# Kernel optimization log

Hardware: AMD Instinct MI355X
Metric: run time of the kernel (lower is better)

## Reference

```python
import jax, jax.numpy as jnp
import numpy as np

EPS = 1e-3
FORGET_BIAS = 1.0


def layer_norm_groups(hmat, n_groups, num_units, gamma, beta):
    # hmat: [B, n_groups*num_units]; normalize each group of num_units independently
    B = hmat.shape[0]
    hr = hmat.reshape(B, n_groups, num_units)
    mean = hr.mean(axis=2, keepdims=True)
    var = ((hr - mean) ** 2).mean(axis=2, keepdims=True)
    hr = (hr - mean) * jax.lax.rsqrt(var + EPS)
    return gamma * hr.reshape(B, n_groups * num_units) + beta


def setup_inputs() -> dict:
    key = jax.random.key(0)
    ks = jax.random.split(key, 5)
    B, I, H = 8192, 1024, 1024
    return {
        "x": jax.random.normal(ks[0], (B, I), jnp.float32),
        "c": jax.random.normal(ks[1], (B, H), jnp.float32),
        "h": jax.random.normal(ks[2], (B, H), jnp.float32),
        "W_xh": jax.random.normal(ks[3], (I, 4 * H), jnp.float32) / np.sqrt(I),
        "W_hh": jax.random.normal(ks[4], (H, 4 * H), jnp.float32) / np.sqrt(H),
        "bias": jnp.zeros((4 * H,), jnp.float32),
        "ln_gamma": jnp.ones((4 * H,), jnp.float32),
        "ln_beta": jnp.zeros((4 * H,), jnp.float32),
        "ln_c_gamma": jnp.ones((H,), jnp.float32),
        "ln_c_beta": jnp.zeros((H,), jnp.float32),
    }


def reference(x, c, h, W_xh, W_hh, bias, ln_gamma, ln_beta, ln_c_gamma, ln_c_beta):
    H = c.shape[1]
    # fused gate matmul: cat([x,h]) @ cat([W_xh,W_hh]) == x@W_xh + h@W_hh
    concat = x @ W_xh + h @ W_hh + bias  # [B, 4H]
    concat = layer_norm_groups(concat, 4, H, ln_gamma, ln_beta)
    i, j, f, o = jnp.split(concat, 4, axis=1)
    new_c = c * jax.nn.sigmoid(f + FORGET_BIAS) + jax.nn.sigmoid(i) * jnp.tanh(j)
    c_ln = layer_norm_groups(new_c, 1, H, ln_c_gamma, ln_c_beta)
    new_h = jnp.tanh(c_ln) * jax.nn.sigmoid(o)
    return new_h, new_c
```

## Files before the change

### kernel.cpp

```cpp
#include <hip/hip_runtime.h>
#include <stdint.h>

#define Mdim 8192
#define Ndim 4096
#define Kdim 2048
#define Hdim 1024

typedef __attribute__((ext_vector_type(8))) short bf16x8;
typedef __attribute__((ext_vector_type(4))) float f32x4;

__device__ __forceinline__ unsigned short f2bf(float f) {
  union { float f; unsigned u; } v; v.f = f;
  unsigned u = v.u + 0x7fffu + ((v.u >> 16) & 1u);
  return (unsigned short)(u >> 16);
}
__device__ __forceinline__ float bf2f(unsigned short s) {
  union { unsigned u; float f; } v; v.u = ((unsigned)s) << 16;
  return v.f;
}
__device__ __forceinline__ float sigmoidf_(float x) { return 1.f / (1.f + __expf(-x)); }
__device__ __forceinline__ float tanhf_(float x) { return 1.f - 2.f / (1.f + __expf(2.f * x)); }

__global__ void conv_a_kernel(const float* __restrict__ x, const float* __restrict__ h,
                              unsigned short* __restrict__ A) {
  int idx = blockIdx.x * 256 + threadIdx.x;
  int m = idx >> 8;
  int k = (idx & 255) * 8;
  const float* src = (k < Hdim) ? (x + (size_t)m * Hdim + k)
                                : (h + (size_t)m * Hdim + (k - Hdim));
  float4 a = ((const float4*)src)[0];
  float4 b = ((const float4*)src)[1];
  union { unsigned short s[8]; int4 v; } o;
  o.s[0] = f2bf(a.x); o.s[1] = f2bf(a.y); o.s[2] = f2bf(a.z); o.s[3] = f2bf(a.w);
  o.s[4] = f2bf(b.x); o.s[5] = f2bf(b.y); o.s[6] = f2bf(b.z); o.s[7] = f2bf(b.w);
  *(int4*)(A + (size_t)idx * 8) = o.v;
}

__global__ void conv_w_kernel(const float* __restrict__ Wxh, const float* __restrict__ Whh,
                              unsigned short* __restrict__ Wt) {
  __shared__ float tile[32][33];
  int k0 = blockIdx.x * 32;
  int n0 = blockIdx.y * 32;
  int tx = threadIdx.x & 31, ty = threadIdx.x >> 5;
#pragma unroll
  for (int i = 0; i < 32; i += 8) {
    int k = k0 + ty + i;
    float v = (k < Hdim) ? Wxh[(size_t)k * Ndim + n0 + tx]
                         : Whh[(size_t)(k - Hdim) * Ndim + n0 + tx];
    tile[ty + i][tx] = v;
  }
  __syncthreads();
#pragma unroll
  for (int i = 0; i < 32; i += 8) {
    int n = n0 + ty + i;
    Wt[(size_t)n * Kdim + k0 + tx] = f2bf(tile[tx][ty + i]);
  }
}

#define BM 128
#define BN 128
#define BK 32
#define NT (Kdim / BK)

__global__ __launch_bounds__(256, 3)
void gemm_kernel(const unsigned short* __restrict__ A, const unsigned short* __restrict__ Bt,
                 unsigned short* __restrict__ C) {
  __shared__ unsigned short lds[2][2][BM * BK];
  int tid = threadIdx.x;
  int bid = blockIdx.x;
  int id = (bid & 7) * 256 + (bid >> 3);
  int mT = id >> 5, nT = id & 31;
  size_t m0 = (size_t)mT * BM, n0 = (size_t)nT * BN;
  int lane = tid & 63, w = tid >> 6;
  int wm = w >> 1, wn = w & 1;
  int q = lane >> 4, r = lane & 15;

  const unsigned short* gA = A + m0 * Kdim;
  const unsigned short* gB = Bt + n0 * Kdim;

  auto stage = [&](int buf, int kt) {
    int k0 = kt * BK;
#pragma unroll
    for (int it = 0; it < 2; ++it) {
      int c = it * 256 + tid;
      int row = c >> 2, slot = c & 3;
      int k8 = slot ^ (row & 3);
      __builtin_amdgcn_global_load_lds(
          (const __attribute__((address_space(1))) void*)(gA + (size_t)row * Kdim + k0 + k8 * 8),
          (__attribute__((address_space(3))) void*)(&lds[buf][0][c * 8]), 16, 0, 0);
      __builtin_amdgcn_global_load_lds(
          (const __attribute__((address_space(1))) void*)(gB + (size_t)row * Kdim + k0 + k8 * 8),
          (__attribute__((address_space(3))) void*)(&lds[buf][1][c * 8]), 16, 0, 0);
    }
  };

  f32x4 acc[4][4] = {};

  stage(0, 0);
  __syncthreads();
  for (int kt = 0; kt < NT; ++kt) {
    int cur = kt & 1;
    if (kt + 1 < NT) stage(cur ^ 1, kt + 1);
    const unsigned short* lA = lds[cur][0];
    const unsigned short* lB = lds[cur][1];
    bf16x8 av[4], bv[4];
    int sl = q ^ (r & 3);
#pragma unroll
    for (int mi = 0; mi < 4; ++mi)
      av[mi] = *(const bf16x8*)(lA + (wm * 64 + mi * 16 + r) * BK + sl * 8);
#pragma unroll
    for (int ni = 0; ni < 4; ++ni)
      bv[ni] = *(const bf16x8*)(lB + (wn * 64 + ni * 16 + r) * BK + sl * 8);
#pragma unroll
    for (int mi = 0; mi < 4; ++mi)
#pragma unroll
      for (int ni = 0; ni < 4; ++ni)
        acc[mi][ni] = __builtin_amdgcn_mfma_f32_16x16x32_bf16(av[mi], bv[ni], acc[mi][ni], 0, 0, 0);
    __syncthreads();
  }

#pragma unroll
  for (int mi = 0; mi < 4; ++mi) {
#pragma unroll
    for (int ni = 0; ni < 4; ++ni) {
      size_t row = m0 + wm * 64 + mi * 16 + q * 4;
      size_t col = n0 + wn * 64 + ni * 16 + r;
#pragma unroll
      for (int j = 0; j < 4; ++j)
        C[(row + j) * Ndim + col] = f2bf(acc[mi][ni][j]);
    }
  }
}

__global__ __launch_bounds__(256)
void tail_kernel(const unsigned short* __restrict__ Cc, const float* __restrict__ cin,
                 const float* __restrict__ bias, const float* __restrict__ gamma,
                 const float* __restrict__ beta, const float* __restrict__ cg,
                 const float* __restrict__ cb, float* __restrict__ out) {
  int lane = threadIdx.x & 63;
  int wid = threadIdx.x >> 6;
  int row = blockIdx.x * 4 + wid;
  const int base = lane * 16;

  const float4* cp = (const float4*)(cin + (size_t)row * Hdim + base);
  float4 c0 = cp[0], c1 = cp[1], c2 = cp[2], c3 = cp[3];
  float cv[16] = {c0.x, c0.y, c0.z, c0.w, c1.x, c1.y, c1.z, c1.w,
                  c2.x, c2.y, c2.z, c2.w, c3.x, c3.y, c3.z, c3.w};

  float accv[16];
  float ov[16];

#pragma unroll
  for (int g = 0; g < 4; ++g) {
    const int4* pp = (const int4*)(Cc + (size_t)row * Ndim + g * Hdim + base);
    int4 u0 = pp[0], u1 = pp[1];
    float vals[16];
    {
      int uu[8] = {u0.x, u0.y, u0.z, u0.w, u1.x, u1.y, u1.z, u1.w};
#pragma unroll
      for (int i = 0; i < 8; ++i) {
        vals[2 * i]     = bf2f((unsigned short)(uu[i] & 0xffff));
        vals[2 * i + 1] = bf2f((unsigned short)(((unsigned)uu[i]) >> 16));
      }
    }
    const float* bp = bias + g * Hdim + base;
#pragma unroll
    for (int t = 0; t < 16; ++t) vals[t] += bp[t];
    float s = 0.f, ss = 0.f;
#pragma unroll
    for (int t = 0; t < 16; ++t) { s += vals[t]; ss += vals[t] * vals[t]; }
#pragma unroll
    for (int off = 32; off; off >>= 1) { s += __shfl_xor(s, off); ss += __shfl_xor(ss, off); }
    float mean = s * (1.f / 1024.f);
    float rstd = rsqrtf(ss * (1.f / 1024.f) - mean * mean + 1e-3f);
    const float* gp = gamma + g * Hdim + base;
    const float* bb = beta + g * Hdim + base;
    if (g == 0) {
#pragma unroll
      for (int t = 0; t < 16; ++t)
        accv[t] = sigmoidf_((vals[t] - mean) * rstd * gp[t] + bb[t]);
    } else if (g == 1) {
#pragma unroll
      for (int t = 0; t < 16; ++t)
        accv[t] *= tanhf_((vals[t] - mean) * rstd * gp[t] + bb[t]);
    } else if (g == 2) {
#pragma unroll
      for (int t = 0; t < 16; ++t)
        accv[t] = cv[t] * sigmoidf_((vals[t] - mean) * rstd * gp[t] + bb[t] + 1.f) + accv[t];
    } else {
#pragma unroll
      for (int t = 0; t < 16; ++t)
        ov[t] = sigmoidf_((vals[t] - mean) * rstd * gp[t] + bb[t]);
    }
  }

  float s = 0.f, ss = 0.f;
#pragma unroll
  for (int t = 0; t < 16; ++t) { s += accv[t]; ss += accv[t] * accv[t]; }
#pragma unroll
  for (int off = 32; off; off >>= 1) { s += __shfl_xor(s, off); ss += __shfl_xor(ss, off); }
  float mean = s * (1.f / 1024.f);
  float rstd = rsqrtf(ss * (1.f / 1024.f) - mean * mean + 1e-3f);

  const float* cgp = cg + base;
  const float* cbp = cb + base;
  float hv[16];
#pragma unroll
  for (int t = 0; t < 16; ++t) {
    float cl = (accv[t] - mean) * rstd * cgp[t] + cbp[t];
    hv[t] = tanhf_(cl) * ov[t];
  }

  float4* oh = (float4*)(out + (size_t)row * Hdim + base);
  float4* oc = (float4*)(out + (size_t)Mdim * Hdim + (size_t)row * Hdim + base);
#pragma unroll
  for (int v = 0; v < 4; ++v) {
    oh[v] = make_float4(hv[4 * v], hv[4 * v + 1], hv[4 * v + 2], hv[4 * v + 3]);
    oc[v] = make_float4(accv[4 * v], accv[4 * v + 1], accv[4 * v + 2], accv[4 * v + 3]);
  }
}

extern "C" void kernel_launch(void* const* d_in, const int* in_sizes, int n_in,
                              void* d_out, int out_size, void* d_ws, size_t ws_size,
                              hipStream_t stream) {
  const float* x    = (const float*)d_in[0];
  const float* c    = (const float*)d_in[1];
  const float* h    = (const float*)d_in[2];
  const float* Wxh  = (const float*)d_in[3];
  const float* Whh  = (const float*)d_in[4];
  const float* bias = (const float*)d_in[5];
  const float* lng  = (const float*)d_in[6];
  const float* lnb  = (const float*)d_in[7];
  const float* cg   = (const float*)d_in[8];
  const float* cb   = (const float*)d_in[9];
  float* out = (float*)d_out;

  unsigned short* Abf = (unsigned short*)d_ws;
  unsigned short* Wt  = Abf + (size_t)Mdim * Kdim;
  unsigned short* Cc  = Wt  + (size_t)Ndim * Kdim;

  conv_a_kernel<<<8192, 256, 0, stream>>>(x, h, Abf);
  conv_w_kernel<<<dim3(Kdim / 32, Ndim / 32), 256, 0, stream>>>(Wxh, Whh, Wt);
  gemm_kernel<<<(Mdim / BM) * (Ndim / BN), 256, 0, stream>>>(Abf, Wt, Cc);
  tail_kernel<<<Mdim / 4, 256, 0, stream>>>(Cc, c, bias, lng, lnb, cg, cb, out);
}
```

Measured before the change: 256.7 us.

## Enlarge GEMM tile to 256x256x64 with 8 waves and interleaved load/MFMA pipeline

Grows the GEMM block tile from 128x128x32 to 256x256x64 and runs it with 512 threads (8 waves). Global-to-LDS staging is split into four quarter regions and interleaved with four MFMA quads per k-step, using barriers, explicit vmcnt waits and s_setprio. The goal is more data reuse per LDS byte and better overlap of memory traffic with matrix math. In exchange it uses more LDS and registers per block and a more fragile hand-written barrier schedule.

```diff
diff --git a/kernel.cpp b/kernel.cpp
--- a/kernel.cpp
+++ b/kernel.cpp
@@ -57,74 +57,148 @@
   }
 }
 
-#define BM 128
-#define BN 128
-#define BK 32
+#define BM 256
+#define BN 256
+#define BK 64
 #define NT (Kdim / BK)
 
-__global__ __launch_bounds__(256, 3)
+__global__ __launch_bounds__(512, 2)
 void gemm_kernel(const unsigned short* __restrict__ A, const unsigned short* __restrict__ Bt,
                  unsigned short* __restrict__ C) {
   __shared__ unsigned short lds[2][2][BM * BK];
-  int tid = threadIdx.x;
+  const int tid = threadIdx.x;
   int bid = blockIdx.x;
-  int id = (bid & 7) * 256 + (bid >> 3);
-  int mT = id >> 5, nT = id & 31;
+  int id = (bid & 7) * 64 + (bid >> 3);
+  int mT = id >> 4, nT = id & 15;
   size_t m0 = (size_t)mT * BM, n0 = (size_t)nT * BN;
-  int lane = tid & 63, w = tid >> 6;
-  int wm = w >> 1, wn = w & 1;
-  int q = lane >> 4, r = lane & 15;
+  const int lane = tid & 63, w = tid >> 6;
+  const int wm = w >> 2, wn = w & 3;
+  const int r16 = lane & 15, q = lane >> 4;
 
   const unsigned short* gA = A + m0 * Kdim;
   const unsigned short* gB = Bt + n0 * Kdim;
 
-  auto stage = [&](int buf, int kt) {
-    int k0 = kt * BK;
+  auto stage = [&](int b, int kt, int region) {
+    const int mat = region >> 1, half = region & 1;
+    const unsigned short* g = mat ? gB : gA;
 #pragma unroll
     for (int it = 0; it < 2; ++it) {
-      int c = it * 256 + tid;
-      int row = c >> 2, slot = c & 3;
-      int k8 = slot ^ (row & 3);
+      int c = it * 512 + tid;
+      int rr = c >> 3, ss = c & 7;
       __builtin_amdgcn_global_load_lds(
-          (const __attribute__((address_space(1))) void*)(gA + (size_t)row * Kdim + k0 + k8 * 8),
-          (__attribute__((address_space(3))) void*)(&lds[buf][0][c * 8]), 16, 0, 0);
-      __builtin_amdgcn_global_load_lds(
-          (const __attribute__((address_space(1))) void*)(gB + (size_t)row * Kdim + k0 + k8 * 8),
-          (__attribute__((address_space(3))) void*)(&lds[buf][1][c * 8]), 16, 0, 0);
+          (const __attribute__((address_space(1))) void*)(
+              g + (size_t)(half * 128 + rr) * Kdim + kt * BK + ((ss ^ (rr & 7)) << 3)),
+          (__attribute__((address_space(3))) void*)(&lds[b][mat][half * (128 * BK) + c * 8]),
+          16, 0, 0);
     }
   };
 
-  f32x4 acc[4][4] = {};
-
-  stage(0, 0);
-  __syncthreads();
-  for (int kt = 0; kt < NT; ++kt) {
-    int cur = kt & 1;
-    if (kt + 1 < NT) stage(cur ^ 1, kt + 1);
-    const unsigned short* lA = lds[cur][0];
-    const unsigned short* lB = lds[cur][1];
-    bf16x8 av[4], bv[4];
-    int sl = q ^ (r & 3);
-#pragma unroll
-    for (int mi = 0; mi < 4; ++mi)
-      av[mi] = *(const bf16x8*)(lA + (wm * 64 + mi * 16 + r) * BK + sl * 8);
-#pragma unroll
-    for (int ni = 0; ni < 4; ++ni)
-      bv[ni] = *(const bf16x8*)(lB + (wn * 64 + ni * 16 + r) * BK + sl * 8);
-#pragma unroll
-    for (int mi = 0; mi < 4; ++mi)
-#pragma unroll
-      for (int ni = 0; ni < 4; ++ni)
-        acc[mi][ni] = __builtin_amdgcn_mfma_f32_16x16x32_bf16(av[mi], bv[ni], acc[mi][ni], 0, 0, 0);
-    __syncthreads();
-  }
-
-#pragma unroll
-  for (int mi = 0; mi < 4; ++mi) {
+  f32x4 acc[8][4] = {};
+  bf16x8 av0[4][2], av1[4][2], bv0[2][2], bv1[2][2];
+
+  auto readA = [&](int cur, int mh, bf16x8 (&av)[4][2]) {
+#pragma unroll
+    for (int mi = 0; mi < 4; ++mi) {
+      int lr = wm * 128 + mh * 64 + mi * 16 + r16;
+      const unsigned short* base = &lds[cur][0][lr * BK];
+#pragma unroll
+      for (int ks = 0; ks < 2; ++ks)
+        av[mi][ks] = *(const bf16x8*)(base + ((((ks << 2) | q) ^ (lr & 7)) << 3));
+    }
+  };
+  auto readB = [&](int cur, int nh, bf16x8 (&bv)[2][2]) {
+#pragma unroll
+    for (int ni = 0; ni < 2; ++ni) {
+      int lr = wn * 64 + nh * 32 + ni * 16 + r16;
+      const unsigned short* base = &lds[cur][1][lr * BK];
+#pragma unroll
+      for (int ks = 0; ks < 2; ++ks)
+        bv[ni][ks] = *(const bf16x8*)(base + ((((ks << 2) | q) ^ (lr & 7)) << 3));
+    }
+  };
+
+#define QUAD(AV, BV, MI0, NI0)                                                        \
+  do {                                                                                \
+    __builtin_amdgcn_s_setprio(1);                                                    \
+    _Pragma("unroll") for (int mi = 0; mi < 4; ++mi)                                  \
+      _Pragma("unroll") for (int ni = 0; ni < 2; ++ni)                                \
+        _Pragma("unroll") for (int ks = 0; ks < 2; ++ks)                              \
+          acc[(MI0) + mi][(NI0) + ni] = __builtin_amdgcn_mfma_f32_16x16x32_bf16(      \
+              AV[mi][ks], BV[ni][ks], acc[(MI0) + mi][(NI0) + ni], 0, 0, 0);          \
+    __builtin_amdgcn_s_setprio(0);                                                    \
+  } while (0)
+
+  stage(0, 0, 0); stage(0, 0, 1); stage(0, 0, 2); stage(0, 0, 3);
+  stage(1, 1, 0); stage(1, 1, 1);
+  asm volatile("s_waitcnt vmcnt(4)" ::: "memory");
+  __builtin_amdgcn_s_barrier();
+
+#pragma unroll 2
+  for (int t = 0; t < NT - 2; ++t) {
+    int cur = t & 1, nxt = cur ^ 1;
+    readA(cur, 0, av0);
+    readB(cur, 0, bv0);
+    stage(nxt, t + 1, 2);
+    __builtin_amdgcn_s_barrier();
+    QUAD(av0, bv0, 0, 0);
+    __builtin_amdgcn_s_barrier();
+    readA(cur, 1, av1);
+    stage(nxt, t + 1, 3);
+    __builtin_amdgcn_s_barrier();
+    QUAD(av1, bv0, 4, 0);
+    __builtin_amdgcn_s_barrier();
+    readB(cur, 1, bv1);
+    stage(cur, t + 2, 0);
+    __builtin_amdgcn_s_barrier();
+    QUAD(av1, bv1, 4, 2);
+    __builtin_amdgcn_s_barrier();
+    stage(cur, t + 2, 1);
+    asm volatile("s_waitcnt vmcnt(4)" ::: "memory");
+    __builtin_amdgcn_s_barrier();
+    QUAD(av0, bv1, 0, 2);
+    __builtin_amdgcn_s_barrier();
+  }
+  {
+    const int cur = (NT - 2) & 1, nxt = cur ^ 1;
+    readA(cur, 0, av0);
+    readB(cur, 0, bv0);
+    stage(nxt, NT - 1, 2);
+    __builtin_amdgcn_s_barrier();
+    QUAD(av0, bv0, 0, 0);
+    __builtin_amdgcn_s_barrier();
+    readA(cur, 1, av1);
+    stage(nxt, NT - 1, 3);
+    __builtin_amdgcn_s_barrier();
+    QUAD(av1, bv0, 4, 0);
+    __builtin_amdgcn_s_barrier();
+    readB(cur, 1, bv1);
+    __builtin_amdgcn_s_barrier();
+    QUAD(av1, bv1, 4, 2);
+    __builtin_amdgcn_s_barrier();
+    asm volatile("s_waitcnt vmcnt(0)" ::: "memory");
+    __builtin_amdgcn_s_barrier();
+    QUAD(av0, bv1, 0, 2);
+    __builtin_amdgcn_s_barrier();
+  }
+  {
+    const int cur = (NT - 1) & 1;
+    readA(cur, 0, av0);
+    readB(cur, 0, bv0);
+    QUAD(av0, bv0, 0, 0);
+    readA(cur, 1, av1);
+    QUAD(av1, bv0, 4, 0);
+    readB(cur, 1, bv1);
+    QUAD(av1, bv1, 4, 2);
+    QUAD(av0, bv1, 0, 2);
+  }
+#undef QUAD
+
+#pragma unroll
+  for (int mi = 0; mi < 8; ++mi) {
 #pragma unroll
     for (int ni = 0; ni < 4; ++ni) {
-      size_t row = m0 + wm * 64 + mi * 16 + q * 4;
-      size_t col = n0 + wn * 64 + ni * 16 + r;
+      size_t row = m0 + wm * 128 + mi * 16 + q * 4;
+      size_t col = n0 + wn * 64 + ni * 16 + r16;
 #pragma unroll
       for (int j = 0; j < 4; ++j)
         C[(row + j) * Ndim + col] = f2bf(acc[mi][ni][j]);
@@ -241,6 +315,6 @@
 
   conv_a_kernel<<<8192, 256, 0, stream>>>(x, h, Abf);
   conv_w_kernel<<<dim3(Kdim / 32, Ndim / 32), 256, 0, stream>>>(Wxh, Whh, Wt);
-  gemm_kernel<<<(Mdim / BM) * (Ndim / BN), 256, 0, stream>>>(Abf, Wt, Cc);
+  gemm_kernel<<<(Mdim / BM) * (Ndim / BN), 512, 0, stream>>>(Abf, Wt, Cc);
   tail_kernel<<<Mdim / 4, 256, 0, stream>>>(Cc, c, bias, lng, lnb, cg, cb, out);
 }
```

After: 214.4 us. 16.5% less time.
